# Performance work log

Measured on AMD Instinct MI355X. Metric: run time of the kernel, lower is better.

The kernel has to match this reference:

```python
import jax, jax.numpy as jnp
import numpy as np

NUM_RBF = 300
RADIUS_RES = 0.1
GAMMA = 10.0
HIDDEN = 64
MB, ATOM = 32, 64


def setup_inputs() -> dict:
    key = jax.random.key(0)
    ks = jax.random.split(key, 12)
    def lin(kw, kb, fan_in, fan_out):
        lim = 1.0 / np.sqrt(fan_in)
        W = jax.random.uniform(kw, (fan_out, fan_in), jnp.float32, -lim, lim)
        b = jax.random.uniform(kb, (fan_out,), jnp.float32, -lim, lim)
        return W, b
    W1, b1 = lin(ks[0], ks[1], HIDDEN, HIDDEN)
    W2, b2 = lin(ks[2], ks[3], HIDDEN, HIDDEN)
    W3, b3 = lin(ks[4], ks[5], HIDDEN, HIDDEN)
    Wd1, bd1 = lin(ks[6], ks[7], NUM_RBF, HIDDEN)
    Wd2, bd2 = lin(ks[8], ks[9], HIDDEN, HIDDEN)
    x = jax.random.normal(ks[10], (MB, ATOM, HIDDEN), jnp.float32)
    dist = jax.random.uniform(ks[11], (MB, ATOM, ATOM), jnp.float32, 0.0, 10.0)
    return {"x": x, "dist": dist,
            "W1": W1, "b1": b1, "W2": W2, "b2": b2, "W3": W3, "b3": b3,
            "Wd1": Wd1, "bd1": bd1, "Wd2": Wd2, "bd2": bd2}


def reference(x, dist, W1, b1, W2, b2, W3, b3, Wd1, bd1, Wd2, bd2):
    sp = jax.nn.softplus
    # linear1 applied per-atom
    v = jnp.einsum('mic,oc->mio', x, W1) + b1                      # [mb, atom, h]
    # CFConv: gaussian RBF expansion of pairwise distances
    centers = jnp.arange(NUM_RBF, dtype=jnp.float32) * RADIUS_RES  # [rbf]
    rbf = jnp.exp(-GAMMA * (dist[..., None] - centers) ** 2)       # [mb, a, a, rbf]
    # 2-layer filter MLP on each pair
    f = sp(jnp.einsum('mijr,hr->mijh', rbf, Wd1) + bd1)            # [mb, a, a, h]
    f = sp(jnp.einsum('mijh,oh->mijo', f, Wd2) + bd2)              # [mb, a, a, h]
    # broadcast-multiply v over pairs and reduce over source atom i (dim=1)
    v = jnp.einsum('mic,mijc->mjc', v, f)                          # [mb, atom, h]
    v = sp(jnp.einsum('mic,oc->mio', v, W2) + b2)
    v = jnp.einsum('mic,oc->mio', v, W3) + b3
    return x + v
```

## Files before the change

### kernel.cpp

```cpp
#include <hip/hip_runtime.h>
#include <math.h>

#define MB_    32
#define ATOM_  64
#define HID_   64
#define NRBF_  300
#define GAMMA_ 10.0f
#define RES_   0.1f

#define TPTS      2001
#define TSTEP     0.005f
#define INV_TSTEP 200.0f

#define RWIN 28

#define T_OFF   0
#define T_SZ    (TPTS * 64)
#define V1_OFF  (T_OFF + T_SZ)
#define V1_SZ   (MB_ * 64 * 64)
#define W2T_OFF (V1_OFF + V1_SZ)
#define W3T_OFF (W2T_OFF + 4096)

__device__ __forceinline__ float sp_f(float x) {
    return fmaxf(x, 0.f) + log1pf(__expf(-fabsf(x)));
}

__global__ __launch_bounds__(256)
void schnet_prep(const float* __restrict__ x,   const float* __restrict__ W1,
                 const float* __restrict__ b1,  const float* __restrict__ W2,
                 const float* __restrict__ W3,  const float* __restrict__ Wd1,
                 const float* __restrict__ bd1, const float* __restrict__ Wd2,
                 const float* __restrict__ bd2, float* __restrict__ ws)
{
    __shared__ float smem[8320];
    const int tid = threadIdx.x;
    const int b   = blockIdx.x;

    if (b < MB_) {
        float* sx = smem;
        float* sw = smem + 4160;
        const float* xm = x + b * 4096;
        for (int e = tid; e < 4096; e += 256) {
            int i = e >> 6, c = e & 63;
            sx[i * 65 + c] = xm[e];
            sw[i * 65 + c] = W1[e];
        }
        __syncthreads();
        const int tx = tid & 15;
        const int ty = tid >> 4;
        float acc[4][4];
        #pragma unroll
        for (int aa = 0; aa < 4; ++aa)
            #pragma unroll
            for (int bb = 0; bb < 4; ++bb)
                acc[aa][bb] = b1[4 * tx + bb];
        #pragma unroll 8
        for (int k = 0; k < 64; ++k) {
            float xa[4], wb[4];
            #pragma unroll
            for (int aa = 0; aa < 4; ++aa) xa[aa] = sx[(4 * ty + aa) * 65 + k];
            #pragma unroll
            for (int bb = 0; bb < 4; ++bb) wb[bb] = sw[(4 * tx + bb) * 65 + k];
            #pragma unroll
            for (int aa = 0; aa < 4; ++aa)
                #pragma unroll
                for (int bb = 0; bb < 4; ++bb)
                    acc[aa][bb] = fmaf(xa[aa], wb[bb], acc[aa][bb]);
        }
        #pragma unroll
        for (int aa = 0; aa < 4; ++aa) {
            float4 v = make_float4(acc[aa][0], acc[aa][1], acc[aa][2], acc[aa][3]);
            *(float4*)(ws + V1_OFF + (b * 64 + 4 * ty + aa) * 64 + 4 * tx) = v;
        }
    } else if (b < MB_ + 501) {
        float* su = smem;
        const int sub = tid >> 6, c = tid & 63;
        const int s  = (b - MB_) * 4 + sub;
        const int se = min(s, TPTS - 1);
        const float d = se * TSTEP;

        int r0 = (int)ceilf((d - 1.35f) * 10.0f);
        r0 = max(r0, 0);

        float a0 = bd1[c], a1 = 0.f;
        const float* wrow1 = Wd1 + c * NRBF_ + r0;
        #pragma unroll
        for (int k = 0; k < RWIN; k += 2) {
            float t0 = fmaf(-RES_, (float)(r0 + k),     d);
            float t1 = fmaf(-RES_, (float)(r0 + k + 1), d);
            float w0 = __expf(-GAMMA_ * t0 * t0);
            float w1 = __expf(-GAMMA_ * t1 * t1);
            a0 = fmaf(w0, wrow1[k],     a0);
            a1 = fmaf(w1, wrow1[k + 1], a1);
        }
        su[sub * 64 + c] = sp_f(a0 + a1);
        __syncthreads();

        const float4* wrow2 = (const float4*)(Wd2 + c * 64);
        const float*  uu    = su + sub * 64;
        float s0 = bd2[c], s1 = 0.f, s2 = 0.f, s3 = 0.f;
        #pragma unroll
        for (int h4 = 0; h4 < 16; ++h4) {
            float4 wv = wrow2[h4];
            s0 = fmaf(wv.x, uu[4 * h4 + 0], s0);
            s1 = fmaf(wv.y, uu[4 * h4 + 1], s1);
            s2 = fmaf(wv.z, uu[4 * h4 + 2], s2);
            s3 = fmaf(wv.w, uu[4 * h4 + 3], s3);
        }
        if (s < TPTS)
            ws[T_OFF + s * 64 + c] = sp_f((s0 + s1) + (s2 + s3));
    } else {
        for (int e = tid; e < 4096; e += 256) {
            int o = e >> 6, c = e & 63;
            ws[W2T_OFF + c * 64 + o] = W2[e];
            ws[W3T_OFF + c * 64 + o] = W3[e];
        }
    }
}

__global__ __launch_bounds__(256)
void schnet_main(const float* __restrict__ x, const float* __restrict__ dist,
                 const float* __restrict__ b2, const float* __restrict__ b3,
                 const float* __restrict__ ws, float* __restrict__ out)
{
    __shared__ float sD[64];
    __shared__ float sRed[4 * 64];
    const int m   = blockIdx.x >> 6;
    const int j   = blockIdx.x & 63;
    const int tid = threadIdx.x;
    const int c   = tid & 63;
    const int p   = tid >> 6;

    if (tid < 64) sD[tid] = dist[(m * ATOM_ + tid) * ATOM_ + j];
    __syncthreads();

    const float* Tb  = ws + T_OFF;
    const float* v1m = ws + V1_OFF + (m * 64 + p * 16) * 64;
    float acc = 0.f;
    #pragma unroll
    for (int ii = 0; ii < 16; ++ii) {
        float d  = sD[p * 16 + ii];
        float f  = d * INV_TSTEP;
        int   s  = min((int)f, TPTS - 2);
        float fr = f - (float)s;
        const float* Tr = Tb + s * 64;
        float t0 = Tr[c], t1 = Tr[64 + c];
        float f2v = fmaf(fr, t1 - t0, t0);
        acc = fmaf(f2v, v1m[ii * 64 + c], acc);
    }
    sRed[p * 64 + c] = acc;
    __syncthreads();
    if (tid < 64)
        sD[tid] = sRed[tid] + sRed[64 + tid] + sRed[128 + tid] + sRed[192 + tid];
    __syncthreads();

    {
        const float* W2t = ws + W2T_OFF;
        float s_ = 0.f;
        #pragma unroll
        for (int cc = 0; cc < 16; ++cc)
            s_ = fmaf(sD[16 * p + cc], W2t[(16 * p + cc) * 64 + c], s_);
        sRed[p * 64 + c] = s_;
    }
    __syncthreads();
    if (tid < 64)
        sD[tid] = sp_f(sRed[tid] + sRed[64 + tid] + sRed[128 + tid] + sRed[192 + tid] + b2[tid]);
    __syncthreads();
    {
        const float* W3t = ws + W3T_OFF;
        float s_ = 0.f;
        #pragma unroll
        for (int cc = 0; cc < 16; ++cc)
            s_ = fmaf(sD[16 * p + cc], W3t[(16 * p + cc) * 64 + c], s_);
        sRed[p * 64 + c] = s_;
    }
    __syncthreads();
    if (tid < 64) {
        float v_ = sRed[tid] + sRed[64 + tid] + sRed[128 + tid] + sRed[192 + tid] + b3[tid];
        out[(m * ATOM_ + j) * HID_ + tid] = v_ + x[(m * ATOM_ + j) * HID_ + tid];
    }
}

extern "C" void kernel_launch(void* const* d_in, const int* in_sizes, int n_in,
                              void* d_out, int out_size, void* d_ws, size_t ws_size,
                              hipStream_t stream) {
    const float* x   = (const float*)d_in[0];
    const float* dist= (const float*)d_in[1];
    const float* W1  = (const float*)d_in[2];
    const float* b1  = (const float*)d_in[3];
    const float* W2  = (const float*)d_in[4];
    const float* b2  = (const float*)d_in[5];
    const float* W3  = (const float*)d_in[6];
    const float* b3  = (const float*)d_in[7];
    const float* Wd1 = (const float*)d_in[8];
    const float* bd1 = (const float*)d_in[9];
    const float* Wd2 = (const float*)d_in[10];
    const float* bd2 = (const float*)d_in[11];
    float* out = (float*)d_out;
    float* ws  = (float*)d_ws;
    (void)in_sizes; (void)n_in; (void)out_size; (void)ws_size;

    schnet_prep<<<dim3(MB_ + 501 + 1), dim3(256), 0, stream>>>(
        x, W1, b1, W2, W3, Wd1, bd1, Wd2, bd2, ws);
    schnet_main<<<dim3(MB_ * ATOM_), dim3(256), 0, stream>>>(
        x, dist, b2, b3, ws, out);
}
```

Baseline: 93.94 us.

## Process four target atoms per block in main kernel, removing cross-wave reductions

The main kernel now assigns four destination atoms j to each block (one per wavefront) instead of one atom split across four waves. Each wave walks all 64 source atoms, so the partial-sum reductions through shared memory and several barriers go away, and the W2/W3 matvecs are done per wave over the full 64 inputs. Distances are loaded as float4 and the grid shrinks by a factor of four. In exchange each thread does four times more serial work and the grid falls to 512 blocks, which lowers parallelism on a many-CU device.

```diff
diff --git a/kernel.cpp b/kernel.cpp
--- a/kernel.cpp
+++ b/kernel.cpp
@@ -123,23 +123,27 @@
                  const float* __restrict__ b2, const float* __restrict__ b3,
                  const float* __restrict__ ws, float* __restrict__ out)
 {
-    __shared__ float sD[64];
-    __shared__ float sRed[4 * 64];
-    const int m   = blockIdx.x >> 6;
-    const int j   = blockIdx.x & 63;
+    __shared__ float sDist[64 * 4];
+    __shared__ float sAgg [4 * 64];
+    __shared__ float sV   [4 * 64];
+    const int m   = blockIdx.x >> 4;
+    const int j0  = (blockIdx.x & 15) * 4;
     const int tid = threadIdx.x;
     const int c   = tid & 63;
     const int p   = tid >> 6;
 
-    if (tid < 64) sD[tid] = dist[(m * ATOM_ + tid) * ATOM_ + j];
+    if (tid < 64) {
+        float4 dv = *(const float4*)(dist + (m * ATOM_ + tid) * ATOM_ + j0);
+        *(float4*)(sDist + tid * 4) = dv;
+    }
     __syncthreads();
 
     const float* Tb  = ws + T_OFF;
-    const float* v1m = ws + V1_OFF + (m * 64 + p * 16) * 64;
+    const float* v1m = ws + V1_OFF + m * 4096;
     float acc = 0.f;
-    #pragma unroll
-    for (int ii = 0; ii < 16; ++ii) {
-        float d  = sD[p * 16 + ii];
+    #pragma unroll 8
+    for (int ii = 0; ii < 64; ++ii) {
+        float d  = sDist[ii * 4 + p];
         float f  = d * INV_TSTEP;
         int   s  = min((int)f, TPTS - 2);
         float fr = f - (float)s;
@@ -148,36 +152,33 @@
         float f2v = fmaf(fr, t1 - t0, t0);
         acc = fmaf(f2v, v1m[ii * 64 + c], acc);
     }
-    sRed[p * 64 + c] = acc;
-    __syncthreads();
-    if (tid < 64)
-        sD[tid] = sRed[tid] + sRed[64 + tid] + sRed[128 + tid] + sRed[192 + tid];
+    sAgg[p * 64 + c] = acc;
     __syncthreads();
 
     {
         const float* W2t = ws + W2T_OFF;
-        float s_ = 0.f;
-        #pragma unroll
-        for (int cc = 0; cc < 16; ++cc)
-            s_ = fmaf(sD[16 * p + cc], W2t[(16 * p + cc) * 64 + c], s_);
-        sRed[p * 64 + c] = s_;
+        const float* ag  = sAgg + p * 64;
+        float s0 = b2[c], s1 = 0.f;
+        #pragma unroll 16
+        for (int cc = 0; cc < 64; cc += 2) {
+            s0 = fmaf(ag[cc],     W2t[cc * 64 + c],       s0);
+            s1 = fmaf(ag[cc + 1], W2t[(cc + 1) * 64 + c], s1);
+        }
+        sV[p * 64 + c] = sp_f(s0 + s1);
     }
     __syncthreads();
-    if (tid < 64)
-        sD[tid] = sp_f(sRed[tid] + sRed[64 + tid] + sRed[128 + tid] + sRed[192 + tid] + b2[tid]);
-    __syncthreads();
+
     {
         const float* W3t = ws + W3T_OFF;
-        float s_ = 0.f;
-        #pragma unroll
-        for (int cc = 0; cc < 16; ++cc)
-            s_ = fmaf(sD[16 * p + cc], W3t[(16 * p + cc) * 64 + c], s_);
-        sRed[p * 64 + c] = s_;
-    }
-    __syncthreads();
-    if (tid < 64) {
-        float v_ = sRed[tid] + sRed[64 + tid] + sRed[128 + tid] + sRed[192 + tid] + b3[tid];
-        out[(m * ATOM_ + j) * HID_ + tid] = v_ + x[(m * ATOM_ + j) * HID_ + tid];
+        const float* vv  = sV + p * 64;
+        float s0 = b3[c], s1 = 0.f;
+        #pragma unroll 16
+        for (int oo = 0; oo < 64; oo += 2) {
+            s0 = fmaf(vv[oo],     W3t[oo * 64 + c],       s0);
+            s1 = fmaf(vv[oo + 1], W3t[(oo + 1) * 64 + c], s1);
+        }
+        const int idx = (m * ATOM_ + j0 + p) * HID_ + c;
+        out[idx] = (s0 + s1) + x[idx];
     }
 }
 
@@ -202,6 +203,6 @@
 
     schnet_prep<<<dim3(MB_ + 501 + 1), dim3(256), 0, stream>>>(
         x, W1, b1, W2, W3, Wd1, bd1, Wd2, bd2, ws);
-    schnet_main<<<dim3(MB_ * ATOM_), dim3(256), 0, stream>>>(
+    schnet_main<<<dim3(MB_ * 16), dim3(256), 0, stream>>>(
         x, dist, b2, b3, ws, out);
 }
```

After: 94.31 us. About the same (+0.4%).
